# Kernel tuning notes

Hardware: AMD Instinct MI355X
Metric: run time of the kernel (lower is better)

Reference implementation:

```python
import jax, jax.numpy as jnp
import numpy as np

B, D_IN, H, HV, A, E, HW = 16384, 512, 512, 256, 32, 8, 512

def _lin(key, fan_in, fan_out):
    k1, k2 = jax.random.split(key)
    s = 1.0 / np.sqrt(fan_in)
    W = jax.random.uniform(k1, (fan_in, fan_out), minval=-s, maxval=s, dtype=jnp.float32)
    b = jax.random.uniform(k2, (fan_out,), minval=-s, maxval=s, dtype=jnp.float32)
    return W, b

def _stack(key, n, fan_in, fan_out):
    Ws, bs = [], []
    for k in jax.random.split(key, n):
        W, b = _lin(k, fan_in, fan_out)
        Ws.append(W); bs.append(b)
    return jnp.stack(Ws), jnp.stack(bs)

def setup_inputs() -> dict:
    key = jax.random.key(0)
    ks = jax.random.split(key, 16)
    x = jax.random.normal(ks[0], (B, D_IN), dtype=jnp.float32)
    # stacked expert policy nets: in->H, H->H, H->A (tanh)
    Wp0, bp0 = _stack(ks[1], E, D_IN, H)
    Wp1, bp1 = _stack(ks[2], E, H, H)
    Wmu, bmu = _stack(ks[3], E, H, A)
    # stacked expert value nets (hardcoded 256 hidden in source): in->256, 256->256, 256->1
    Wv0, bv0 = _stack(ks[4], E, D_IN, HV)
    Wv1, bv1 = _stack(ks[5], E, HV, HV)
    Wv, bv = _stack(ks[6], E, HV, 1)
    # gating net: in->HW, HW->HW, HW->E, softmax
    Ww0, bw0 = _lin(ks[7], D_IN, HW)
    Ww1, bw1 = _lin(ks[8], HW, HW)
    Wwo, bwo = _lin(ks[9], HW, E)
    return dict(x=x, Wp0=Wp0, bp0=bp0, Wp1=Wp1, bp1=bp1, Wmu=Wmu, bmu=bmu,
                Wv0=Wv0, bv0=bv0, Wv1=Wv1, bv1=bv1, Wv=Wv, bv=bv,
                Ww0=Ww0, bw0=bw0, Ww1=Ww1, bw1=bw1, Wwo=Wwo, bwo=bwo)

def reference(x, Wp0, bp0, Wp1, bp1, Wmu, bmu, Wv0, bv0, Wv1, bv1, Wv, bv,
              Ww0, bw0, Ww1, bw1, Wwo, bwo):
    # experts as one grouped/batched GEMM over axis e
    h = jax.nn.relu(jnp.einsum('bi,eih->ebh', x, Wp0) + bp0[:, None, :])      # [E,B,H]
    h = jax.nn.relu(jnp.einsum('ebh,ehk->ebk', h, Wp1) + bp1[:, None, :])
    actions = jnp.tanh(jnp.einsum('ebh,eha->eba', h, Wmu) + bmu[:, None, :])  # [E,B,A]
    # per-expert values
    g = jax.nn.relu(jnp.einsum('bi,eih->ebh', x, Wv0) + bv0[:, None, :])      # [E,B,HV]
    g = jax.nn.relu(jnp.einsum('ebh,ehk->ebk', g, Wv1) + bv1[:, None, :])
    values = jnp.einsum('ebh,eho->ebo', g, Wv) + bv[:, None, :]               # [E,B,1]
    # gating network + softmax
    u = jax.nn.relu(x @ Ww0 + bw0)
    u = jax.nn.relu(u @ Ww1 + bw1)
    w = jax.nn.softmax(u @ Wwo + bwo, axis=-1)                                # [B,E]
    # Categorical(w).sample() with a fixed key, then per-row gather of values
    pis = jax.random.categorical(jax.random.key(42), jnp.log(w), axis=-1)     # [B] int
    v = values[pis, jnp.arange(values.shape[1])]                              # [B,1]
    return actions, v, w
```

## Files before the change

### kernel.cpp

```cpp
#include <hip/hip_runtime.h>


typedef float   f32x4 __attribute__((ext_vector_type(4)));
typedef _Float16 f16;
typedef _Float16 f16x4 __attribute__((ext_vector_type(4)));
typedef _Float16 f16x8 __attribute__((ext_vector_type(8)));

typedef __attribute__((address_space(1))) unsigned int gas_u32;
typedef __attribute__((address_space(3))) unsigned int las_u32;

__device__ __forceinline__ void gl_lds16(const void* g, void* l) {
  __builtin_amdgcn_global_load_lds((gas_u32*)g, (las_u32*)l, 16, 0, 0);
}

__device__ __forceinline__ int xcd_swz(int b, int G) {
  int q = G >> 3, r = G & 7;
  int x = b & 7, y = b >> 3;
  return (x < r ? x * (q + 1) : r * (q + 1) + (x - r) * q) + y;
}

template<int EPI>
__global__ __launch_bounds__(512, 4) void gemm3_kernel(
    const f16* __restrict__ A, const f16* __restrict__ BT,
    const float* __restrict__ bias, void* __restrict__ Cv,
    const int K, const int lda, const int ldc,
    const long long sAe, const long long sCe,
    const int mT, const int nInner, const int eShift)
{
  constexpr int BM = 256, BN = 128;
  __shared__ __align__(16) char sm[(BM + BN) * 128];
  char* Ash = sm;
  char* Bsh = sm + BM * 128;

  const int tid = threadIdx.x;
  const int lane = tid & 63;
  const int wid = tid >> 6;
  const int wr = wid >> 1, wc = wid & 1;

  const int L = xcd_swz(blockIdx.x, gridDim.x);
  const int nIn = L % nInner;
  const int m = (L / nInner) % mT;
  const int eo = L / (nInner * mT);
  const int nv0 = (eo * nInner + nIn) * BN;
  const int e = nv0 >> eShift;
  const int col0 = nv0 & ((1 << eShift) - 1);
  const int m0 = m * BM;

  const f16* Ab = A + (size_t)sAe * e + (size_t)m0 * lda;
  const f16* Bb = BT + (size_t)nv0 * K;

  f32x4 acc[4][4] = {};
  const int ksteps = K >> 6;

  for (int kt = 0; kt < ksteps; ++kt) {
    __syncthreads();
    const f16* Ak = Ab + (kt << 6);
    const f16* Bk = Bb + (kt << 6);
    #pragma unroll
    for (int u0 = 0; u0 < BM * 8; u0 += 512) {
      int u = u0 + tid;
      int row = u >> 3;
      int kb = ((u & 7) << 4) ^ ((row & 7) << 4);
      gl_lds16(Ak + (size_t)row * lda + (kb >> 1), Ash + u * 16);
    }
    #pragma unroll
    for (int u0 = 0; u0 < BN * 8; u0 += 512) {
      int u = u0 + tid;
      int row = u >> 3;
      int kb = ((u & 7) << 4) ^ ((row & 7) << 4);
      gl_lds16(Bk + (size_t)row * K + (kb >> 1), Bsh + u * 16);
    }
    __syncthreads();

    f16x8 af[4][2], bf[4][2];
    const int kl = (lane >> 4) << 4;
    #pragma unroll
    for (int fm = 0; fm < 4; ++fm) {
      int row = wr * 64 + fm * 16 + (lane & 15);
      int sw = (row & 7) << 4;
      af[fm][0] = *(const f16x8*)(Ash + row * 128 + (kl ^ sw));
      af[fm][1] = *(const f16x8*)(Ash + row * 128 + ((64 + kl) ^ sw));
    }
    #pragma unroll
    for (int fn = 0; fn < 4; ++fn) {
      int row = wc * 64 + fn * 16 + (lane & 15);
      int sw = (row & 7) << 4;
      bf[fn][0] = *(const f16x8*)(Bsh + row * 128 + (kl ^ sw));
      bf[fn][1] = *(const f16x8*)(Bsh + row * 128 + ((64 + kl) ^ sw));
    }
    #pragma unroll
    for (int fm = 0; fm < 4; ++fm)
      #pragma unroll
      for (int fn = 0; fn < 4; ++fn) {
        acc[fm][fn] = __builtin_amdgcn_mfma_f32_16x16x32_f16(
            bf[fn][0], af[fm][0], acc[fm][fn], 0, 0, 0);
        acc[fm][fn] = __builtin_amdgcn_mfma_f32_16x16x32_f16(
            bf[fn][1], af[fm][1], acc[fm][fn], 0, 0, 0);
      }
  }

  const int rbase = m0 + wr * 64 + (lane & 15);
  const int cb = wc * 64 + ((lane >> 4) << 2);
  #pragma unroll
  for (int fm = 0; fm < 4; ++fm) {
    const int row = rbase + fm * 16;
    #pragma unroll
    for (int fn = 0; fn < 4; ++fn) {
      const int bcol = cb + fn * 16;
      const int col = col0 + bcol;
      f32x4 v = acc[fm][fn];
      f32x4 bb = *(const f32x4*)(bias + nv0 + bcol);
      f16x4 h;
      #pragma unroll
      for (int r = 0; r < 4; ++r) h[r] = (f16)fmaxf(v[r] + bb[r], 0.0f);
      *(f16x4*)((f16*)Cv + (size_t)sCe * e + (size_t)row * ldc + col) = h;
    }
  }
}

template<int BM, int BN, int WM, int WN, int EPI>
__global__ __launch_bounds__(256, 2) void gemm2_kernel(
    const f16* __restrict__ A, const f16* __restrict__ BT,
    const float* __restrict__ bias, void* __restrict__ Cv,
    const int K, const int lda, const int ldc,
    const long long sAe, const long long sCe,
    const int mT, const int nInner, const int eShift)
{
  constexpr int FM = WM / 16, FN = WN / 16;
  constexpr int WAVES_N = BN / WN;
  __shared__ __align__(16) char sm[(BM + BN) * 128];
  char* Ash = sm;
  char* Bsh = sm + BM * 128;

  const int tid = threadIdx.x;
  const int lane = tid & 63;
  const int wid = tid >> 6;

  const int L = xcd_swz(blockIdx.x, gridDim.x);
  const int nIn = L % nInner;
  const int m = (L / nInner) % mT;
  const int eo = L / (nInner * mT);
  const int nv0 = (eo * nInner + nIn) * BN;
  const int e = nv0 >> eShift;
  const int col0 = nv0 & ((1 << eShift) - 1);
  const int m0 = m * BM;

  const f16* Ab = A + (size_t)sAe * e + (size_t)m0 * lda;
  const f16* Bb = BT + (size_t)nv0 * K;
  const int wr = wid / WAVES_N, wc = wid % WAVES_N;

  f32x4 acc[FM][FN] = {};
  const int ksteps = K >> 6;

  for (int kt = 0; kt < ksteps; ++kt) {
    __syncthreads();
    const f16* Ak = Ab + (kt << 6);
    const f16* Bk = Bb + (kt << 6);
    for (int u0 = 0; u0 < BM * 8; u0 += 256) {
      int u = u0 + tid;
      int row = u >> 3;
      int kb = ((u & 7) << 4) ^ ((row & 7) << 4);
      gl_lds16(Ak + (size_t)row * lda + (kb >> 1), Ash + u * 16);
    }
    for (int u0 = 0; u0 < BN * 8; u0 += 256) {
      int u = u0 + tid;
      int row = u >> 3;
      int kb = ((u & 7) << 4) ^ ((row & 7) << 4);
      gl_lds16(Bk + (size_t)row * K + (kb >> 1), Bsh + u * 16);
    }
    __syncthreads();

    f16x8 af[FM][2], bf[FN][2];
    const int kl = (lane >> 4) << 4;
    #pragma unroll
    for (int fm = 0; fm < FM; ++fm) {
      int row = wr * WM + fm * 16 + (lane & 15);
      int sw = (row & 7) << 4;
      af[fm][0] = *(const f16x8*)(Ash + row * 128 + (kl ^ sw));
      af[fm][1] = *(const f16x8*)(Ash + row * 128 + ((64 + kl) ^ sw));
    }
    #pragma unroll
    for (int fn = 0; fn < FN; ++fn) {
      int row = wc * WN + fn * 16 + (lane & 15);
      int sw = (row & 7) << 4;
      bf[fn][0] = *(const f16x8*)(Bsh + row * 128 + (kl ^ sw));
      bf[fn][1] = *(const f16x8*)(Bsh + row * 128 + ((64 + kl) ^ sw));
    }
    #pragma unroll
    for (int fm = 0; fm < FM; ++fm)
      #pragma unroll
      for (int fn = 0; fn < FN; ++fn) {
        acc[fm][fn] = __builtin_amdgcn_mfma_f32_16x16x32_f16(
            bf[fn][0], af[fm][0], acc[fm][fn], 0, 0, 0);
        acc[fm][fn] = __builtin_amdgcn_mfma_f32_16x16x32_f16(
            bf[fn][1], af[fm][1], acc[fm][fn], 0, 0, 0);
      }
  }

  const int rbase = m0 + wr * WM + (lane & 15);
  const int cb = wc * WN + ((lane >> 4) << 2);
  #pragma unroll
  for (int fm = 0; fm < FM; ++fm) {
    const int row = rbase + fm * 16;
    #pragma unroll
    for (int fn = 0; fn < FN; ++fn) {
      const int bcol = cb + fn * 16;
      const int col = col0 + bcol;
      f32x4 v = acc[fm][fn];
      f32x4 bb = *(const f32x4*)(bias + nv0 + bcol);
      if constexpr (EPI == 1) {
        f32x4 o;
        #pragma unroll
        for (int r = 0; r < 4; ++r) o[r] = tanhf(v[r] + bb[r]);
        *(f32x4*)((float*)Cv + (size_t)sCe * e + (size_t)row * ldc + col) = o;
      } else if constexpr (EPI == 2) {
        f32x4 o;
        #pragma unroll
        for (int r = 0; r < 4; ++r) o[r] = fmaxf(v[r] + bb[r], 0.0f);
        *(f32x4*)((float*)Cv + (size_t)sCe * e + (size_t)row * ldc + col) = o;
      } else {
        f16x4 h, l, s;
        #pragma unroll
        for (int r = 0; r < 4; ++r) {
          float u = fmaxf(v[r] + bb[r], 0.0f);
          f16 hh = (f16)u;
          float hv = (float)hh;
          h[r] = hh;
          l[r] = (f16)((u - hv) * 32.0f);
          s[r] = (f16)(hv * 0.03125f);
        }
        f16* cp = (f16*)Cv + (size_t)sCe * e + (size_t)row * ldc + col;
        *(f16x4*)(cp) = h;
        *(f16x4*)(cp + 512) = l;
        *(f16x4*)(cp + 1024) = s;
      }
    }
  }
}

__global__ __launch_bounds__(256) void prep_kernel(
    const float* __restrict__ x, f16* __restrict__ xsplit,
    const float* __restrict__ Wp0, f16* __restrict__ Wp0T,
    const float* __restrict__ Wp1, f16* __restrict__ Wp1T,
    const float* __restrict__ Wmu, f16* __restrict__ WmuT,
    const float* __restrict__ Wv0, f16* __restrict__ Wv0T,
    const float* __restrict__ Wv1, f16* __restrict__ Wv1T,
    const float* __restrict__ Ww0, f16* __restrict__ Ww0T3,
    const float* __restrict__ Ww1, f16* __restrict__ Ww1T3)
{
  __shared__ float t[32][33];
  const int tid = threadIdx.x;
  int b = blockIdx.x;
  if (b < 8192) {
    const size_t i = ((size_t)b * 256 + tid) * 4;
    const int row = (int)(i >> 9);
    const int col = (int)(i & 511);
    f32x4 v = *(const f32x4*)(x + i);
    f16x4 h, l, s;
    #pragma unroll
    for (int j = 0; j < 4; ++j) {
      f16 hh = (f16)v[j];
      float hv = (float)hh;
      h[j] = hh;
      l[j] = (f16)((v[j] - hv) * 32.0f);
      s[j] = (f16)(hv * 0.03125f);
    }
    f16* p = xsplit + (size_t)row * 1536 + col;
    *(f16x4*)(p) = h;
    *(f16x4*)(p + 512) = l;
    *(f16x4*)(p + 1024) = s;
    return;
  }
  b -= 8192;
  const float* W;
  f16* T;
  bool triple = false;
  int K, N;
  if (b < 2048)               { W = Wp0; T = Wp0T; K = 512; N = 512; }
  else if ((b -= 2048) < 2048){ W = Wp1; T = Wp1T; K = 512; N = 512; }
  else if ((b -= 2048) < 128) { W = Wmu; T = WmuT; K = 512; N = 32; }
  else if ((b -= 128) < 1024) { W = Wv0; T = Wv0T; K = 512; N = 256; }
  else if ((b -= 1024) < 512) { W = Wv1; T = Wv1T; K = 256; N = 256; }
  else if ((b -= 512) < 256)  { W = Ww0; T = Ww0T3; triple = true; K = 512; N = 512; }
  else { b -= 256;              W = Ww1; T = Ww1T3; triple = true; K = 512; N = 512; }

  const int kT = K >> 5, nT = N >> 5;
  const int e = b / (kT * nT);
  const int rem = b % (kT * nT);
  const int k0 = (rem % kT) << 5;
  const int n0 = (rem / kT) << 5;
  const int tx = tid & 31, ty = tid >> 5;
  const float* Wp = W + (size_t)e * K * N;
  #pragma unroll
  for (int i = 0; i < 4; ++i)
    t[ty + i * 8][tx] = Wp[(size_t)(k0 + ty + i * 8) * N + n0 + tx];
  __syncthreads();
  #pragma unroll
  for (int i = 0; i < 4; ++i) {
    const int n = n0 + ty + i * 8, k = k0 + tx;
    float v = t[tx][ty + i * 8];
    f16 hh = (f16)v;
    if (!triple) {
      T[(size_t)e * K * N + (size_t)n * K + k] = hh;
    } else {
      float hv = (float)hh;
      f16* p = T + (size_t)n * 1536 + k;
      p[0] = hh;
      p[512] = (f16)(hv * 0.03125f);
      p[1024] = (f16)((v - hv) * 32.0f);
    }
  }
}

__global__ __launch_bounds__(256) void values_kernel(
    const f16* __restrict__ G2, const float* __restrict__ Wv,
    const float* __restrict__ bv, float* __restrict__ values, const int e0)
{
  const int tid = threadIdx.x, lane = tid & 63, wid = tid >> 6;
  const int gi = blockIdx.x * 4 + wid;
  const int el = gi >> 14;
  const int b = gi & 16383;
  const int eg = e0 + el;
  const f16* g = G2 + (((size_t)el << 14) + b) * 256 + (lane << 2);
  f16x4 gv = *(const f16x4*)g;
  const float* wv = Wv + ((size_t)eg << 8) + (lane << 2);
  float a = (float)gv[0] * wv[0] + (float)gv[1] * wv[1] +
            (float)gv[2] * wv[2] + (float)gv[3] * wv[3];
  #pragma unroll
  for (int off = 32; off >= 1; off >>= 1) a += __shfl_xor(a, off);
  if (lane == 0) values[((size_t)eg << 14) + b] = a + bv[eg];
}

__device__ __forceinline__ void threefry_0_42(unsigned x0, unsigned x1,
                                              unsigned& o0, unsigned& o1)
{
  const unsigned ks0 = 0u, ks1 = 42u, ks2 = 0x1BD11BDAu ^ 42u;
  x0 += ks0; x1 += ks1;
#define TF_R(r) { x0 += x1; x1 = (x1 << r) | (x1 >> (32 - r)); x1 ^= x0; }
  TF_R(13) TF_R(15) TF_R(26) TF_R(6)  x0 += ks1; x1 += ks2 + 1u;
  TF_R(17) TF_R(29) TF_R(16) TF_R(24) x0 += ks2; x1 += ks0 + 2u;
  TF_R(13) TF_R(15) TF_R(26) TF_R(6)  x0 += ks0; x1 += ks1 + 3u;
  TF_R(17) TF_R(29) TF_R(16) TF_R(24) x0 += ks1; x1 += ks2 + 4u;
  TF_R(13) TF_R(15) TF_R(26) TF_R(6)  x0 += ks2; x1 += ks0 + 5u;
#undef TF_R
  o0 = x0; o1 = x1;
}

__global__ __launch_bounds__(256) void gating_out_kernel(
    const float* __restrict__ U2, const float* __restrict__ Wwo,
    const float* __restrict__ bwo, const float* __restrict__ values,
    float* __restrict__ w_out, float* __restrict__ v_out)
{
  __shared__ float wl[4096];
  const int tid = threadIdx.x;
  for (int i = tid; i < 1024; i += 256)
    ((f32x4*)wl)[i] = ((const f32x4*)Wwo)[i];
  __syncthreads();
  const int lane = tid & 63, wid = tid >> 6;
  const int b = blockIdx.x * 4 + wid;

  const float* u = U2 + (size_t)b * 512 + lane * 8;
  f32x4 ua = *(const f32x4*)u;
  f32x4 ub = *(const f32x4*)(u + 4);
  float acc[8] = {};
  const float* wrow = wl + lane * 64;
  #pragma unroll
  for (int i = 0; i < 8; ++i) {
    float uv = (i < 4) ? ua[i] : ub[i - 4];
    #pragma unroll
    for (int ee = 0; ee < 8; ++ee) acc[ee] += uv * wrow[i * 8 + ee];
  }
  #pragma unroll
  for (int off = 32; off >= 1; off >>= 1)
    #pragma unroll
    for (int ee = 0; ee < 8; ++ee) acc[ee] += __shfl_xor(acc[ee], off);
  #pragma unroll
  for (int ee = 0; ee < 8; ++ee) acc[ee] += bwo[ee];

  float zmax = acc[0];
  #pragma unroll
  for (int ee = 1; ee < 8; ++ee) zmax = fmaxf(zmax, acc[ee]);
  float s = 0.0f;
  #pragma unroll
  for (int ee = 0; ee < 8; ++ee) s += expf(acc[ee] - zmax);

  float t0 = (lane & 1) ? acc[1] : acc[0];
  float t1 = (lane & 1) ? acc[3] : acc[2];
  float t2 = (lane & 1) ? acc[5] : acc[4];
  float t3 = (lane & 1) ? acc[7] : acc[6];
  float s0 = (lane & 2) ? t1 : t0;
  float s1 = (lane & 2) ? t3 : t2;
  float zown = (lane & 4) ? s1 : s0;

  if (lane < 8) w_out[(size_t)b * 8 + lane] = expf(zown - zmax) / s;

  unsigned idx = ((unsigned)b << 3) | (unsigned)(lane & 7);
  unsigned o0, o1;
  threefry_0_42(0u, idx, o0, o1);
  unsigned bits = o0 ^ o1;
  float f = __uint_as_float((bits >> 9) | 0x3F800000u) - 1.0f;
  f = fmaxf(f, 1.17549435e-38f);
  float g = -logf(-logf(f));
  float y = (lane < 8) ? (zown + g) : -3.0e38f;

  float best = __shfl(y, 0);
  int pi = 0;
  #pragma unroll
  for (int ee = 1; ee < 8; ++ee) {
    float ye = __shfl(y, ee);
    if (ye > best) { best = ye; pi = ee; }
  }
  if (lane == 0) v_out[b] = values[((size_t)pi << 14) + b];
}

extern "C" void kernel_launch(void* const* d_in, const int* in_sizes, int n_in,
                              void* d_out, int out_size, void* d_ws, size_t ws_size,
                              hipStream_t stream) {
  (void)in_sizes; (void)n_in; (void)out_size; (void)ws_size;
  const float* x   = (const float*)d_in[0];
  const float* Wp0 = (const float*)d_in[1];
  const float* bp0 = (const float*)d_in[2];
  const float* Wp1 = (const float*)d_in[3];
  const float* bp1 = (const float*)d_in[4];
  const float* Wmu = (const float*)d_in[5];
  const float* bmu = (const float*)d_in[6];
  const float* Wv0 = (const float*)d_in[7];
  const float* bv0 = (const float*)d_in[8];
  const float* Wv1 = (const float*)d_in[9];
  const float* bv1 = (const float*)d_in[10];
  const float* Wv  = (const float*)d_in[11];
  const float* bv  = (const float*)d_in[12];
  const float* Ww0 = (const float*)d_in[13];
  const float* bw0 = (const float*)d_in[14];
  const float* Ww1 = (const float*)d_in[15];
  const float* bw1 = (const float*)d_in[16];
  const float* Wwo = (const float*)d_in[17];
  const float* bwo = (const float*)d_in[18];

  float* out_actions = (float*)d_out;
  float* out_v = out_actions + (size_t)8 * 16384 * 32;
  float* out_w = out_v + 16384;

  char* base = (char*)d_ws;
  size_t off = 0;
  auto alloc = [&](size_t bytes) -> char* {
    char* p = base + off;
    off = (off + bytes + 255) & ~(size_t)255;
    return p;
  };

  f16* xsplit = (f16*)alloc((size_t)16384 * 1536 * 2);
  f16* Wp0T   = (f16*)alloc((size_t)8 * 512 * 512 * 2);
  f16* Wp1T   = (f16*)alloc((size_t)8 * 512 * 512 * 2);
  f16* WmuT   = (f16*)alloc((size_t)8 * 32 * 512 * 2);
  f16* Wv0T   = (f16*)alloc((size_t)8 * 256 * 512 * 2);
  f16* Wv1T   = (f16*)alloc((size_t)8 * 256 * 256 * 2);
  f16* Ww0T3  = (f16*)alloc((size_t)512 * 1536 * 2);
  f16* Ww1T3  = (f16*)alloc((size_t)512 * 1536 * 2);
  float* valuesBuf = (float*)alloc((size_t)8 * 16384 * 4);

  char* arena = base + off;
  const size_t SZ67 = (size_t)67108864;
  f16* P1 = (f16*)arena;
  f16* P2 = (f16*)(arena + SZ67);
  f16* VB1 = (f16*)arena;
  f16* VB2 = (f16*)(arena + SZ67);
  f16* U1split = (f16*)arena;
  float* U2 = (float*)(arena + (size_t)50331648);

  dim3 blk(256);
  dim3 blk8(512);
  const long long sBD = 16384LL * 512;
  const long long sBH = 16384LL * 256;

  prep_kernel<<<14464, blk, 0, stream>>>(
      x, xsplit, Wp0, Wp0T, Wp1, Wp1T, Wmu, WmuT, Wv0, Wv0T, Wv1, Wv1T,
      Ww0, Ww0T3, Ww1, Ww1T3);

  for (int e0 = 0; e0 < 8; e0 += 4) {
    gemm3_kernel<0><<<1024, blk8, 0, stream>>>(
        xsplit, Wp0T + (size_t)e0 * 512 * 512, bp0 + e0 * 512, P1,
        512, 1536, 512, 0, sBD, 64, 16, 9);
    gemm3_kernel<0><<<1024, blk8, 0, stream>>>(
        P1, Wp1T + (size_t)e0 * 512 * 512, bp1 + e0 * 512, P2,
        512, 512, 512, sBD, sBD, 64, 4, 9);
    gemm2_kernel<128, 32, 32, 32, 1><<<512, blk, 0, stream>>>(
        P2, WmuT + (size_t)e0 * 32 * 512, bmu + e0 * 32,
        out_actions + (size_t)e0 * 16384 * 32,
        512, 512, 32, sBD, 16384LL * 32, 128, 1, 5);
  }

  gemm3_kernel<0><<<1024, blk8, 0, stream>>>(
      xsplit, Wv0T, bv0, VB1, 512, 1536, 256, 0, sBH, 64, 16, 8);
  gemm3_kernel<0><<<1024, blk8, 0, stream>>>(
      VB1, Wv1T, bv1, VB2, 256, 256, 256, sBH, sBH, 64, 2, 8);
  values_kernel<<<32768, blk, 0, stream>>>((const f16*)VB2, Wv, bv, valuesBuf, 0);

  gemm2_kernel<128, 128, 64, 64, 3><<<512, blk, 0, stream>>>(
      xsplit, Ww0T3, bw0, U1split, 1536, 1536, 1536, 0, 0, 128, 4, 9);
  gemm2_kernel<128, 128, 64, 64, 2><<<512, blk, 0, stream>>>(
      U1split, Ww1T3, bw1, U2, 1536, 1536, 512, 0, 0, 128, 4, 9);
  gating_out_kernel<<<4096, blk, 0, stream>>>(U2, Wwo, bwo, valuesBuf, out_w, out_v);
}
```

Before: 461.8 us.

## Fuse value-head dot product into second value GEMM epilogue with atomics

The second value-net GEMM now computes relu(acc+bias) and immediately dots it with the value-head weights, reducing across lanes and atomically accumulating per-row partial sums into a zeroed values buffer. This removes writing the full hidden activation tensor to memory, the separate values kernel that reread it, and one launch. The bias bv is added later in the gating output kernel. The change adds a memset and floating-point atomics, which make the summation order nondeterministic.

```diff
diff --git a/kernel.cpp b/kernel.cpp
--- a/kernel.cpp
+++ b/kernel.cpp
@@ -25,7 +25,8 @@
     const float* __restrict__ bias, void* __restrict__ Cv,
     const int K, const int lda, const int ldc,
     const long long sAe, const long long sCe,
-    const int mT, const int nInner, const int eShift)
+    const int mT, const int nInner, const int eShift,
+    const float* __restrict__ Wv, float* __restrict__ values)
 {
   constexpr int BM = 256, BN = 128;
   __shared__ __align__(16) char sm[(BM + BN) * 128];
@@ -101,6 +102,29 @@
 
   const int rbase = m0 + wr * 64 + (lane & 15);
   const int cb = wc * 64 + ((lane >> 4) << 2);
+
+  if constexpr (EPI == 4) {
+    #pragma unroll
+    for (int fm = 0; fm < 4; ++fm) {
+      const int row = rbase + fm * 16;
+      float s = 0.0f;
+      #pragma unroll
+      for (int fn = 0; fn < 4; ++fn) {
+        const int bcol = cb + fn * 16;
+        const int col = col0 + bcol;
+        f32x4 v = acc[fm][fn];
+        f32x4 bb = *(const f32x4*)(bias + nv0 + bcol);
+        #pragma unroll
+        for (int r = 0; r < 4; ++r)
+          s += fmaxf(v[r] + bb[r], 0.0f) * Wv[(e << 8) + col + r];
+      }
+      s += __shfl_xor(s, 16);
+      s += __shfl_xor(s, 32);
+      if (lane < 16) atomicAdd(&values[((size_t)e << 14) + row], s);
+    }
+    return;
+  }
+
   #pragma unroll
   for (int fm = 0; fm < 4; ++fm) {
     const int row = rbase + fm * 16;
@@ -312,25 +336,6 @@
   }
 }
 
-__global__ __launch_bounds__(256) void values_kernel(
-    const f16* __restrict__ G2, const float* __restrict__ Wv,
-    const float* __restrict__ bv, float* __restrict__ values, const int e0)
-{
-  const int tid = threadIdx.x, lane = tid & 63, wid = tid >> 6;
-  const int gi = blockIdx.x * 4 + wid;
-  const int el = gi >> 14;
-  const int b = gi & 16383;
-  const int eg = e0 + el;
-  const f16* g = G2 + (((size_t)el << 14) + b) * 256 + (lane << 2);
-  f16x4 gv = *(const f16x4*)g;
-  const float* wv = Wv + ((size_t)eg << 8) + (lane << 2);
-  float a = (float)gv[0] * wv[0] + (float)gv[1] * wv[1] +
-            (float)gv[2] * wv[2] + (float)gv[3] * wv[3];
-  #pragma unroll
-  for (int off = 32; off >= 1; off >>= 1) a += __shfl_xor(a, off);
-  if (lane == 0) values[((size_t)eg << 14) + b] = a + bv[eg];
-}
-
 __device__ __forceinline__ void threefry_0_42(unsigned x0, unsigned x1,
                                               unsigned& o0, unsigned& o1)
 {
@@ -349,6 +354,7 @@
 __global__ __launch_bounds__(256) void gating_out_kernel(
     const float* __restrict__ U2, const float* __restrict__ Wwo,
     const float* __restrict__ bwo, const float* __restrict__ values,
+    const float* __restrict__ bv,
     float* __restrict__ w_out, float* __restrict__ v_out)
 {
   __shared__ float wl[4096];
@@ -410,7 +416,7 @@
     float ye = __shfl(y, ee);
     if (ye > best) { best = ye; pi = ee; }
   }
-  if (lane == 0) v_out[b] = values[((size_t)pi << 14) + b];
+  if (lane == 0) v_out[b] = values[((size_t)pi << 14) + b] + bv[pi];
 }
 
 extern "C" void kernel_launch(void* const* d_in, const int* in_sizes, int n_in,
@@ -464,7 +470,6 @@
   f16* P1 = (f16*)arena;
   f16* P2 = (f16*)(arena + SZ67);
   f16* VB1 = (f16*)arena;
-  f16* VB2 = (f16*)(arena + SZ67);
   f16* U1split = (f16*)arena;
   float* U2 = (float*)(arena + (size_t)50331648);
 
@@ -480,10 +485,10 @@
   for (int e0 = 0; e0 < 8; e0 += 4) {
     gemm3_kernel<0><<<1024, blk8, 0, stream>>>(
         xsplit, Wp0T + (size_t)e0 * 512 * 512, bp0 + e0 * 512, P1,
-        512, 1536, 512, 0, sBD, 64, 16, 9);
+        512, 1536, 512, 0, sBD, 64, 16, 9, nullptr, nullptr);
     gemm3_kernel<0><<<1024, blk8, 0, stream>>>(
         P1, Wp1T + (size_t)e0 * 512 * 512, bp1 + e0 * 512, P2,
-        512, 512, 512, sBD, sBD, 64, 4, 9);
+        512, 512, 512, sBD, sBD, 64, 4, 9, nullptr, nullptr);
     gemm2_kernel<128, 32, 32, 32, 1><<<512, blk, 0, stream>>>(
         P2, WmuT + (size_t)e0 * 32 * 512, bmu + e0 * 32,
         out_actions + (size_t)e0 * 16384 * 32,
@@ -491,14 +496,17 @@
   }
 
   gemm3_kernel<0><<<1024, blk8, 0, stream>>>(
-      xsplit, Wv0T, bv0, VB1, 512, 1536, 256, 0, sBH, 64, 16, 8);
-  gemm3_kernel<0><<<1024, blk8, 0, stream>>>(
-      VB1, Wv1T, bv1, VB2, 256, 256, 256, sBH, sBH, 64, 2, 8);
-  values_kernel<<<32768, blk, 0, stream>>>((const f16*)VB2, Wv, bv, valuesBuf, 0);
+      xsplit, Wv0T, bv0, VB1, 512, 1536, 256, 0, sBH, 64, 16, 8,
+      nullptr, nullptr);
+  hipMemsetAsync(valuesBuf, 0, (size_t)8 * 16384 * 4, stream);
+  gemm3_kernel<4><<<1024, blk8, 0, stream>>>(
+      VB1, Wv1T, bv1, nullptr, 256, 256, 256, sBH, 0, 64, 2, 8,
+      Wv, valuesBuf);
 
   gemm2_kernel<128, 128, 64, 64, 3><<<512, blk, 0, stream>>>(
       xsplit, Ww0T3, bw0, U1split, 1536, 1536, 1536, 0, 0, 128, 4, 9);
   gemm2_kernel<128, 128, 64, 64, 2><<<512, blk, 0, stream>>>(
       U1split, Ww1T3, bw1, U2, 1536, 1536, 512, 0, 0, 128, 4, 9);
-  gating_out_kernel<<<4096, blk, 0, stream>>>(U2, Wwo, bwo, valuesBuf, out_w, out_v);
-}
+  gating_out_kernel<<<4096, blk, 0, stream>>>(
+      U2, Wwo, bwo, valuesBuf, bv, out_w, out_v);
+}
```

New measurement: 426.0 us (median of 2 runs). 1.08x faster.
